# Kernel tuning notes

Measured on AMD Instinct MI355X. Metric: run time of the kernel, lower is better.

## Reference

```python
import jax, jax.numpy as jnp
import numpy as np

N_NODES = 100000
N_EDGES = 1600000
D_FEAT = 64
D_HID = 128
N_HOP = 3


def setup_inputs() -> dict:
    key = jax.random.key(0)
    ks = jax.random.split(key, 7)
    nodes = jax.random.normal(ks[0], (N_NODES, D_FEAT), dtype=jnp.float32)
    senders = jax.random.randint(ks[1], (N_EDGES,), 0, N_NODES, dtype=jnp.int32)
    receivers = jax.random.randint(ks[2], (N_EDGES,), 0, N_NODES, dtype=jnp.int32)
    # per-hop MLP params (n_hop=3 independent layers), lecun-style scaling
    W1 = jax.random.normal(ks[3], (N_HOP, D_FEAT, D_HID), dtype=jnp.float32) / np.sqrt(D_FEAT)
    b1 = jnp.zeros((N_HOP, D_HID), dtype=jnp.float32)
    W2 = jax.random.normal(ks[4], (N_HOP, D_HID, D_FEAT), dtype=jnp.float32) / np.sqrt(D_HID)
    b2 = jnp.zeros((N_HOP, D_FEAT), dtype=jnp.float32)
    return {"nodes": nodes, "senders": senders, "receivers": receivers,
            "W1": W1, "b1": b1, "W2": W2, "b2": b2}


def _gcn_hop(x, senders, receivers, w1, b1, w2, b2):
    # update_node_fn: 2-layer MLP with leaky_relu between layers
    x = jax.nn.leaky_relu(jnp.dot(x, w1) + b1)
    x = jnp.dot(x, w2) + b2
    n = x.shape[0]
    ones = jnp.ones(senders.shape, dtype=x.dtype)
    send_deg = jax.ops.segment_sum(ones, senders, num_segments=n)
    recv_deg = jax.ops.segment_sum(ones, receivers, num_segments=n)
    # symmetric normalization: D_s^{-1/2} gather -> scatter-sum -> D_r^{-1/2}
    x = x * jax.lax.rsqrt(jnp.maximum(send_deg, 1.0))[:, None]
    x = jax.ops.segment_sum(x[senders], receivers, num_segments=n)
    x = x * jax.lax.rsqrt(jnp.maximum(recv_deg, 1.0))[:, None]
    return x


def reference(nodes, senders, receivers, W1, b1, W2, b2):
    x = nodes
    for i in range(N_HOP):
        x = _gcn_hop(x, senders, receivers, W1[i], b1[i], W2[i], b2[i])
    return x
```

## Files before the change

kernel.cpp:

```cpp
#include <hip/hip_runtime.h>

#define LRELU_SLOPE 0.01f
#define NBLK_A 512
#define BIN_SZ 256
#define MAXBIN 5120
#define NC2 128

typedef unsigned short ushort_t;
typedef unsigned int uint_t;

typedef float f32x4 __attribute__((ext_vector_type(4)));
typedef short bf16x8 __attribute__((ext_vector_type(8)));
#define MFMA16(a, b, c) __builtin_amdgcn_mfma_f32_16x16x32_bf16(a, b, c, 0, 0, 0)

__device__ inline uint_t f2bf(float f) {
    unsigned u = __float_as_uint(f);
    return (u + 0x7FFFu + ((u >> 16) & 1u)) >> 16;
}

__device__ inline void split2(float v, uint_t& hi, uint_t& lo) {
    hi = f2bf(v);
    float hif = __uint_as_float(hi << 16);
    lo = f2bf(v - hif);
}

__device__ inline float4 bf4_to_f4(ushort4 v) {
    float4 r;
    r.x = __uint_as_float((unsigned)v.x << 16);
    r.y = __uint_as_float((unsigned)v.y << 16);
    r.z = __uint_as_float((unsigned)v.z << 16);
    r.w = __uint_as_float((unsigned)v.w << 16);
    return r;
}

__device__ inline void acc_bf8(uint4 v, float* a) {
    a[0] += __uint_as_float(v.x << 16);
    a[1] += __uint_as_float(v.x & 0xFFFF0000u);
    a[2] += __uint_as_float(v.y << 16);
    a[3] += __uint_as_float(v.y & 0xFFFF0000u);
    a[4] += __uint_as_float(v.z << 16);
    a[5] += __uint_as_float(v.z & 0xFFFF0000u);
    a[6] += __uint_as_float(v.w << 16);
    a[7] += __uint_as_float(v.w & 0xFFFF0000u);
}

__device__ inline void acc_bf8m(uint4 v, float ok, float* a) {
    a[0] = fmaf(__uint_as_float(v.x << 16), ok, a[0]);
    a[1] = fmaf(__uint_as_float(v.x & 0xFFFF0000u), ok, a[1]);
    a[2] = fmaf(__uint_as_float(v.y << 16), ok, a[2]);
    a[3] = fmaf(__uint_as_float(v.y & 0xFFFF0000u), ok, a[3]);
    a[4] = fmaf(__uint_as_float(v.z << 16), ok, a[4]);
    a[5] = fmaf(__uint_as_float(v.z & 0xFFFF0000u), ok, a[5]);
    a[6] = fmaf(__uint_as_float(v.w << 16), ok, a[6]);
    a[7] = fmaf(__uint_as_float(v.w & 0xFFFF0000u), ok, a[7]);
}


__global__ __launch_bounds__(256) void binhist_kernel(const int* __restrict__ keys,
        int* __restrict__ cntA, int cs, int e, int nbins) {
    __shared__ int cnt[512];
    int b = blockIdx.x, t = threadIdx.x;
    for (int i = t; i < nbins; i += 256) cnt[i] = 0;
    __syncthreads();
    int base = b * cs, lim = min(cs, e - base);
    for (int i = t; i < lim; i += 256)
        atomicAdd(&cnt[keys[base + i] >> 8], 1);
    __syncthreads();
    for (int i = t; i < nbins; i += 256) cntA[b * nbins + i] = cnt[i];
}

__global__ __launch_bounds__(512) void binoffA_kernel(const int* __restrict__ cntA,
        int* __restrict__ offT, int* __restrict__ binTot, int nbins) {
    __shared__ int s[NBLK_A];
    int bin = blockIdx.x, t = threadIdx.x;
    int v = cntA[t * nbins + bin];
    s[t] = v;
    __syncthreads();
    for (int off = 1; off < NBLK_A; off <<= 1) {
        int add = (t >= off) ? s[t - off] : 0;
        __syncthreads();
        s[t] += add;
        __syncthreads();
    }
    offT[bin * NBLK_A + t] = s[t] - v;
    if (t == NBLK_A - 1) binTot[bin] = s[t];
}

__global__ __launch_bounds__(512) void scanb_kernel(const int* __restrict__ binTot,
        int* __restrict__ binStart, int nbins) {
    __shared__ int s[512];
    int t = threadIdx.x;
    int v = (t < nbins) ? binTot[t] : 0;
    s[t] = v;
    __syncthreads();
    for (int off = 1; off < 512; off <<= 1) {
        int add = (t >= off) ? s[t - off] : 0;
        __syncthreads();
        s[t] += add;
        __syncthreads();
    }
    if (t < nbins) binStart[t] = s[t] - v;
    if (t == nbins - 1) binStart[nbins] = s[t];
}

__global__ __launch_bounds__(256) void binscat_kernel(const int* __restrict__ keys,
        const int* __restrict__ payload, const int* __restrict__ offT,
        const int* __restrict__ binStart,
        uint2* __restrict__ pairs, int cs, int e, int nbins) {
    __shared__ int cur[512];
    int b = blockIdx.x, t = threadIdx.x;
    for (int i = t; i < nbins; i += 256) cur[i] = offT[i * NBLK_A + b] + binStart[i];
    __syncthreads();
    int base = b * cs, lim = min(cs, e - base);
    for (int i = t; i < lim; i += 256) {
        int k = keys[base + i];
        int pl = payload[base + i];
        int pos = atomicAdd(&cur[k >> 8], 1);
        pairs[pos] = make_uint2((unsigned)k, (unsigned)pl);
    }
}

__global__ __launch_bounds__(256) void binsort_kernel(const uint2* __restrict__ pairs,
        const int* __restrict__ binStart, int* __restrict__ row_start,
        int* __restrict__ bucket, int nbins, int n, int e) {
    __shared__ int cnt[BIN_SZ];
    __shared__ int loc[BIN_SZ];
    __shared__ int buf[MAXBIN];
    int bin = blockIdx.x, t = threadIdx.x;
    int e0 = binStart[bin], e1 = binStart[bin + 1];
    int m = e1 - e0;
    if (m > MAXBIN) m = MAXBIN;
    cnt[t] = 0;
    __syncthreads();
    for (int i = t; i < m; i += 256)
        atomicAdd(&cnt[pairs[e0 + i].x & 255], 1);
    __syncthreads();
    int v = cnt[t];
    int node = bin * BIN_SZ + t;
    loc[t] = v;
    __syncthreads();
    for (int off = 1; off < BIN_SZ; off <<= 1) {
        int add = (t >= off) ? loc[t - off] : 0;
        __syncthreads();
        loc[t] += add;
        __syncthreads();
    }
    int excl = loc[t] - v;
    if (node < n) row_start[node] = e0 + excl;
    if (bin == nbins - 1 && t == 255) row_start[n] = e;
    cnt[t] = excl;
    __syncthreads();
    for (int i = t; i < m; i += 256) {
        uint2 pr = pairs[e0 + i];
        int pos = atomicAdd(&cnt[pr.x & 255], 1);
        buf[pos] = (int)pr.y;
    }
    __syncthreads();
    for (int i = t; i < m; i += 256) bucket[e0 + i] = buf[i];
}


__global__ __launch_bounds__(256) void hist8v2_kernel(const int* __restrict__ keys,
        uint_t* __restrict__ hist, int cs, int e, int half, int nwords) {
    __shared__ uint_t lds[12500];
    int c = blockIdx.x >> 1;
    int h = blockIdx.x & 1;
    int t = threadIdx.x;
    int hw = half >> 2;
    for (int i = t; i < hw; i += 256) lds[i] = 0;
    __syncthreads();
    int base = c * cs, lim = min(cs, e - base);
    int lo = h * half;
    for (int i = t; i < lim; i += 256) {
        int v = keys[base + i] - lo;
        if ((unsigned)v < (unsigned)half)
            atomicAdd(&lds[v >> 2], 1u << ((v & 3) * 8));
    }
    __syncthreads();
    uint_t* d = hist + (size_t)c * nwords + (size_t)h * hw;
    for (int i = t; i < hw; i += 256) d[i] = lds[i];
}

__global__ __launch_bounds__(256) void scancv2_kernel(const uint_t* __restrict__ hist,
        int* __restrict__ deg, int nwords, int n) {
    int w = blockIdx.x * 256 + threadIdx.x;
    if (w >= nwords) return;
    uint_t run = 0;
    for (int c = 0; c < NC2; c++) run += hist[(size_t)c * nwords + w];
    int v = w * 4;
    if (v + 3 < n) {
        ((int4*)deg)[w] = make_int4(run & 255, (run >> 8) & 255,
                                    (run >> 16) & 255, (int)(run >> 24));
    } else {
        for (int j = 0; j < 4 && v + j < n; j++) deg[v + j] = (run >> (8 * j)) & 255;
    }
}


__global__ __launch_bounds__(256) void prep_w_kernel(const float* __restrict__ W1,
        const float* __restrict__ W2, ushort_t* __restrict__ w1p, ushort_t* __restrict__ w2p) {
    int hop = blockIdx.x;
    const float* w1 = W1 + hop * 64 * 128;
    const float* w2 = W2 + hop * 128 * 64;
    ushort_t* p1h = w1p + (size_t)hop * 16384;
    ushort_t* p1l = p1h + 8192;
    ushort_t* p2h = w2p + (size_t)hop * 16384;
    ushort_t* p2l = p2h + 8192;
    for (int i = threadIdx.x; i < 8192; i += 256) {
        int j = i & 7, o = (i >> 3) & 127, cq = i >> 10;
        int k = (cq >> 2) * 32 + (cq & 3) * 8 + j;
        uint_t h, l;
        split2(w1[k * 128 + o], h, l);
        p1h[i] = (ushort_t)h; p1l[i] = (ushort_t)l;
    }
    for (int i = threadIdx.x; i < 8192; i += 256) {
        int j = i & 7, o = (i >> 3) & 63, cq = i >> 9;
        int k = (cq >> 2) * 32 + (cq & 3) * 8 + j;
        uint_t h, l;
        split2(w2[k * 64 + o], h, l);
        p2h[i] = (ushort_t)h; p2l[i] = (ushort_t)l;
    }
}


template<int GATHER>
__global__ __launch_bounds__(512) void fused_mlp_kernel(const float* __restrict__ x,
        const ushort_t* __restrict__ yin, const int* __restrict__ rs,
        const int* __restrict__ bucket,
        const ushort_t* __restrict__ w1p, const float* __restrict__ b1g,
        const ushort_t* __restrict__ w2p, const float* __restrict__ b2g,
        const int* __restrict__ sdeg, ushort_t* __restrict__ y, int n) {
    __shared__ __align__(16) char smem[54272];
    ushort_t* xsh = (ushort_t*)smem;
    ushort_t* xsl = xsh + 4608;
    ushort_t* hsh = xsl + 4608;
    ushort_t* hsl = hsh + 8704;
    float* b1f   = (float*)(hsl + 8704);
    float* b2f   = b1f + 128;
    float* snorm = b2f + 64;
    float* ybuf  = (float*)smem;

    const ushort_t* w1ph = w1p;
    const ushort_t* w1pl = w1p + 8192;
    const ushort_t* w2ph = w2p;
    const ushort_t* w2pl = w2p + 8192;

    int tid = threadIdx.x;
    int nb = blockIdx.x * 64;

    if (tid < 32) ((float4*)b1f)[tid] = ((const float4*)b1g)[tid];
    else if (tid < 48) ((float4*)b2f)[tid - 32] = ((const float4*)b2g)[tid - 32];
    if (tid >= 448) {
        int t = tid - 448;
        int gn = nb + t;
        int d = (gn < n) ? sdeg[gn] : 1;
        snorm[t] = rsqrtf(fmaxf((float)d, 1.0f));
    }

    if (GATHER) {
        int node = tid >> 3, j = tid & 7;
        int gn = nb + node;
        float a[8];
        #pragma unroll
        for (int k = 0; k < 8; k++) a[k] = 0.f;
        if (gn < n) {
            int s0 = rs[gn];
            int deg = rs[gn + 1] - s0;
            const uint4* yrow = (const uint4*)yin;
            int i = 0;
            for (; i + 16 <= deg; i += 16) {
                int idx[16];
                #pragma unroll
                for (int k = 0; k < 16; k++) idx[k] = bucket[s0 + i + k];
                uint4 r0[16];
                #pragma unroll
                for (int k = 0; k < 16; k++) r0[k] = yrow[(size_t)idx[k] * 8 + j];
                #pragma unroll
                for (int k = 0; k < 16; k++) acc_bf8(r0[k], a);
            }
            for (; i < deg; i += 8) {
                int idx[8]; float ok[8];
                #pragma unroll
                for (int k = 0; k < 8; k++) {
                    int ii = i + k;
                    bool v = ii < deg;
                    idx[k] = bucket[v ? s0 + ii : s0];
                    ok[k] = v ? 1.0f : 0.0f;
                }
                uint4 rr[8];
                #pragma unroll
                for (int k = 0; k < 8; k++) rr[k] = yrow[(size_t)idx[k] * 8 + j];
                #pragma unroll
                for (int k = 0; k < 8; k++) acc_bf8m(rr[k], ok[k], a);
            }
            float sc = rsqrtf(fmaxf((float)deg, 1.0f));
            #pragma unroll
            for (int k = 0; k < 8; k++) a[k] *= sc;
        }
        uint_t h[8], l[8];
        #pragma unroll
        for (int k = 0; k < 8; k++) split2(a[k], h[k], l[k]);
        uint4 oh, ol;
        oh.x = h[0] | (h[1] << 16); oh.y = h[2] | (h[3] << 16);
        oh.z = h[4] | (h[5] << 16); oh.w = h[6] | (h[7] << 16);
        ol.x = l[0] | (l[1] << 16); ol.y = l[2] | (l[3] << 16);
        ol.z = l[4] | (l[5] << 16); ol.w = l[6] | (l[7] << 16);
        *(uint4*)&xsh[node * 72 + j * 8] = oh;
        *(uint4*)&xsl[node * 72 + j * 8] = ol;
    } else {
        for (int i = tid; i < 1024; i += 512) {
            int node = i >> 4, c4 = i & 15;
            int gn = nb + node;
            float4 v = make_float4(0.f, 0.f, 0.f, 0.f);
            if (gn < n) v = ((const float4*)x)[(size_t)gn * 16 + c4];
            uint_t h0, l0, h1, l1, h2, l2, h3, l3;
            split2(v.x, h0, l0); split2(v.y, h1, l1);
            split2(v.z, h2, l2); split2(v.w, h3, l3);
            *(uint2*)&xsh[node * 72 + c4 * 4] = make_uint2(h0 | (h1 << 16), h2 | (h3 << 16));
            *(uint2*)&xsl[node * 72 + c4 * 4] = make_uint2(l0 | (l1 << 16), l2 | (l3 << 16));
        }
    }
    __syncthreads();

    int w = tid >> 6, lane = tid & 63;
    int q = lane >> 4, m = lane & 15;
    int oq = w & 3, nh = w >> 2;
    bool even = ((m & 1) == 0);

    {
        f32x4 acc[2][2];
        #pragma unroll
        for (int a = 0; a < 2; a++)
            #pragma unroll
            for (int b = 0; b < 2; b++) acc[a][b] = (f32x4)(0.f);

        #pragma unroll
        for (int c = 0; c < 2; c++) {
            bf16x8 Ah[2], Al[2];
            #pragma unroll
            for (int nt = 0; nt < 2; nt++) {
                int node = nh * 32 + nt * 16 + m;
                Ah[nt] = *(const bf16x8*)&xsh[node * 72 + c * 32 + q * 8];
                Al[nt] = *(const bf16x8*)&xsl[node * 72 + c * 32 + q * 8];
            }
            #pragma unroll
            for (int ot = 0; ot < 2; ot++) {
                int o1 = oq * 32 + ot * 16 + m;
                size_t fo = (size_t)((c * 4 + q) * 128 + o1) * 8;
                bf16x8 Bh = *(const bf16x8*)&w1ph[fo];
                bf16x8 Bl = *(const bf16x8*)&w1pl[fo];
                #pragma unroll
                for (int nt = 0; nt < 2; nt++) {
                    acc[ot][nt] = MFMA16(Ah[nt], Bh, acc[ot][nt]);
                    acc[ot][nt] = MFMA16(Ah[nt], Bl, acc[ot][nt]);
                    acc[ot][nt] = MFMA16(Al[nt], Bh, acc[ot][nt]);
                }
            }
        }
        float b1v[2];
        b1v[0] = b1f[oq * 32 + m];
        b1v[1] = b1f[oq * 32 + 16 + m];
        #pragma unroll
        for (int ot = 0; ot < 2; ot++)
            #pragma unroll
            for (int nt = 0; nt < 2; nt++) {
                float hv[4], pv[4];
                #pragma unroll
                for (int r = 0; r < 4; r++) {
                    float t = acc[ot][nt][r] + b1v[ot];
                    hv[r] = (t > 0.f) ? t : LRELU_SLOPE * t;
                }
                #pragma unroll
                for (int r = 0; r < 4; r++) pv[r] = __shfl_xor(hv[r], 1, 64);
                int kpos = oq * 32 + ot * 16 + (m & ~1);
                #pragma unroll
                for (int rr = 0; rr < 2; rr++) {
                    int r = even ? rr : (2 + rr);
                    float vlo = even ? hv[r] : pv[r];
                    float vhi = even ? pv[r] : hv[r];
                    uint_t ah, al, bh, bl;
                    split2(vlo, ah, al);
                    split2(vhi, bh, bl);
                    int node = nh * 32 + nt * 16 + 4 * q + r;
                    *(uint_t*)&hsh[node * 136 + kpos] = ah | (bh << 16);
                    *(uint_t*)&hsl[node * 136 + kpos] = al | (bl << 16);
                }
            }
    }
    __syncthreads();

    {
        int ot2 = oq;
        f32x4 acc2[2];
        acc2[0] = (f32x4)(0.f);
        acc2[1] = (f32x4)(0.f);
        #pragma unroll
        for (int c = 0; c < 4; c++) {
            int o2 = ot2 * 16 + m;
            size_t fo = (size_t)((c * 4 + q) * 64 + o2) * 8;
            bf16x8 Bh = *(const bf16x8*)&w2ph[fo];
            bf16x8 Bl = *(const bf16x8*)&w2pl[fo];
            #pragma unroll
            for (int nt = 0; nt < 2; nt++) {
                int node = nh * 32 + nt * 16 + m;
                bf16x8 Ah = *(const bf16x8*)&hsh[node * 136 + c * 32 + q * 8];
                bf16x8 Al = *(const bf16x8*)&hsl[node * 136 + c * 32 + q * 8];
                acc2[nt] = MFMA16(Ah, Bh, acc2[nt]);
                acc2[nt] = MFMA16(Ah, Bl, acc2[nt]);
                acc2[nt] = MFMA16(Al, Bh, acc2[nt]);
            }
        }
        float b2v = b2f[ot2 * 16 + m];
        #pragma unroll
        for (int nt = 0; nt < 2; nt++)
            #pragma unroll
            for (int r = 0; r < 4; r++) {
                int node = nh * 32 + nt * 16 + 4 * q + r;
                float sn = snorm[node];
                ybuf[node * 68 + ot2 * 16 + m] = (acc2[nt][r] + b2v) * sn;
            }
    }
    __syncthreads();

    {
        int node = tid >> 3, c8 = tid & 7;
        int gn = nb + node;
        if (gn < n) {
            const float* src = &ybuf[node * 68 + c8 * 8];
            float4 v0 = *(const float4*)src;
            float4 v1 = *(const float4*)(src + 4);
            uint4 o;
            o.x = f2bf(v0.x) | (f2bf(v0.y) << 16);
            o.y = f2bf(v0.z) | (f2bf(v0.w) << 16);
            o.z = f2bf(v1.x) | (f2bf(v1.y) << 16);
            o.w = f2bf(v1.z) | (f2bf(v1.w) << 16);
            ((uint4*)y)[(size_t)gn * 8 + c8] = o;
        }
    }
}


__global__ __launch_bounds__(256) void agg_kernel(const ushort_t* __restrict__ y,
        const int* __restrict__ rs, const int* __restrict__ bucket,
        float* __restrict__ dst, int n) {
    int wid  = (blockIdx.x * 256 + threadIdx.x) >> 6;
    int lane = threadIdx.x & 63;
    int nd   = lane >> 5;
    int slot = (lane >> 4) & 1;
    int f4   = lane & 15;
    int node = wid * 2 + nd;
    if (node >= n) return;
    int s0  = rs[node];
    int deg = rs[node + 1] - s0;
    const ushort4* y4 = (const ushort4*)y;
    float4 acc = make_float4(0.f, 0.f, 0.f, 0.f);
    for (int i = slot; i < deg; i += 16) {
        int idx[8]; float ok[8];
        #pragma unroll
        for (int j = 0; j < 8; j++) {
            int ii = i + 2 * j;
            bool v = ii < deg;
            idx[j] = bucket[v ? s0 + ii : s0];
            ok[j] = v ? 1.0f : 0.0f;
        }
        #pragma unroll
        for (int j = 0; j < 8; j++) {
            float4 v4 = bf4_to_f4(y4[(size_t)idx[j] * 16 + f4]);
            acc.x = fmaf(v4.x, ok[j], acc.x);
            acc.y = fmaf(v4.y, ok[j], acc.y);
            acc.z = fmaf(v4.z, ok[j], acc.z);
            acc.w = fmaf(v4.w, ok[j], acc.w);
        }
    }
    acc.x += __shfl_xor(acc.x, 16, 64);
    acc.y += __shfl_xor(acc.y, 16, 64);
    acc.z += __shfl_xor(acc.z, 16, 64);
    acc.w += __shfl_xor(acc.w, 16, 64);
    if (slot == 0) {
        float sc = rsqrtf(fmaxf((float)deg, 1.0f));
        acc.x *= sc; acc.y *= sc; acc.z *= sc; acc.w *= sc;
        ((float4*)dst)[(size_t)node * 16 + f4] = acc;
    }
}


extern "C" void kernel_launch(void* const* d_in, const int* in_sizes, int n_in,
                              void* d_out, int out_size, void* d_ws, size_t ws_size,
                              hipStream_t stream) {
    const float* nodes     = (const float*)d_in[0];
    const int*   senders   = (const int*)d_in[1];
    const int*   receivers = (const int*)d_in[2];
    const float* W1 = (const float*)d_in[3];
    const float* b1 = (const float*)d_in[4];
    const float* W2 = (const float*)d_in[5];
    const float* b2 = (const float*)d_in[6];

    int N = in_sizes[0] / 64;
    int E = in_sizes[1];
    int NBINS = (N + BIN_SZ - 1) / BIN_SZ;
    int CSA = (E + NBLK_A - 1) / NBLK_A;
    int CS2 = (E + NC2 - 1) / NC2;
    int HALF = ((N + 7) / 8) * 4;
    int NW2 = 2 * (HALF >> 2);

    char* p = (char*)d_ws;
    auto carve = [&](size_t bytes) -> char* {
        char* r = p;
        p += (bytes + 255) & ~(size_t)255;
        return r;
    };
    ushort_t* yA   = (ushort_t*)carve((size_t)N * 64 * 2);
    ushort_t* yB   = (ushort_t*)carve((size_t)N * 64 * 2);
    int*      rs   = (int*)carve((size_t)(N + 1) * 4);
    int*      sdeg = (int*)carve((size_t)N * 4);
    int*      bucket = (int*)carve((size_t)E * 4);
    int*      binStart = (int*)carve((size_t)(NBINS + 1) * 4);
    int*      binTot   = (int*)carve((size_t)NBINS * 4);
    ushort_t* w1p  = (ushort_t*)carve((size_t)3 * 16384 * 2);
    ushort_t* w2p  = (ushort_t*)carve((size_t)3 * 16384 * 2);
    char* scratch  = carve((size_t)E * 8 + 2 * (size_t)NBLK_A * NBINS * 4 + 4096);
    uint2* pairs = (uint2*)scratch;
    int*   cntA  = (int*)(scratch + (size_t)E * 8);
    int*   offT  = cntA + (size_t)NBLK_A * NBINS;
    uint_t* T1   = (uint_t*)pairs;

    prep_w_kernel<<<3, 256, 0, stream>>>(W1, W2, w1p, w2p);
    binhist_kernel<<<NBLK_A, 256, 0, stream>>>(receivers, cntA, CSA, E, NBINS);
    binoffA_kernel<<<NBINS, NBLK_A, 0, stream>>>(cntA, offT, binTot, NBINS);
    scanb_kernel<<<1, 512, 0, stream>>>(binTot, binStart, NBINS);
    binscat_kernel<<<NBLK_A, 256, 0, stream>>>(receivers, senders, offT, binStart, pairs, CSA, E, NBINS);
    binsort_kernel<<<NBINS, 256, 0, stream>>>(pairs, binStart, rs, bucket, NBINS, N, E);
    hist8v2_kernel<<<NC2 * 2, 256, 0, stream>>>(senders, T1, CS2, E, HALF, NW2);
    scancv2_kernel<<<(NW2 + 255) / 256, 256, 0, stream>>>(T1, sdeg, NW2, N);

    int mbf = (N + 63) / 64;
    int agg_blocks = (N / 2 + 4) / 4 + 1;

    fused_mlp_kernel<0><<<mbf, 512, 0, stream>>>(nodes, nullptr, nullptr, nullptr,
            w1p, b1, w2p, b2, sdeg, yA, N);
    fused_mlp_kernel<1><<<mbf, 512, 0, stream>>>(nullptr, yA, rs, bucket,
            w1p + 16384, b1 + 128, w2p + 16384, b2 + 64, sdeg, yB, N);
    fused_mlp_kernel<1><<<mbf, 512, 0, stream>>>(nullptr, yB, rs, bucket,
            w1p + 32768, b1 + 256, w2p + 32768, b2 + 128, sdeg, yA, N);
    agg_kernel<<<agg_blocks, 256, 0, stream>>>(yA, rs, bucket, (float*)d_out, N);
}
```

Baseline: 358.1 us.

## Merge preprocessing kernels and software-pipeline gather with MLP over two node tiles

The weight-prep, receiver bin histogram and sender degree histogram kernels are merged into one launch, and the bin-offset scan and degree reduction into a second, which cuts the number of small launches. The gather+MLP hops now run in a new kernel that handles two 64-node tiles per block. The first 16 neighbour rows of the second tile are prefetched while the first tile's MFMA work runs, so gather latency overlaps with compute. This raises register pressure (the 16 prefetched uint4 registers) and halves the grid size, with launch bounds set to 4 blocks.

```diff
diff --git a/kernel.cpp b/kernel.cpp
--- a/kernel.cpp
+++ b/kernel.cpp
@@ -56,34 +56,100 @@
 }
 
 
-__global__ __launch_bounds__(256) void binhist_kernel(const int* __restrict__ keys,
-        int* __restrict__ cntA, int cs, int e, int nbins) {
-    __shared__ int cnt[512];
-    int b = blockIdx.x, t = threadIdx.x;
-    for (int i = t; i < nbins; i += 256) cnt[i] = 0;
-    __syncthreads();
-    int base = b * cs, lim = min(cs, e - base);
-    for (int i = t; i < lim; i += 256)
-        atomicAdd(&cnt[keys[base + i] >> 8], 1);
-    __syncthreads();
-    for (int i = t; i < nbins; i += 256) cntA[b * nbins + i] = cnt[i];
-}
-
-__global__ __launch_bounds__(512) void binoffA_kernel(const int* __restrict__ cntA,
-        int* __restrict__ offT, int* __restrict__ binTot, int nbins) {
+__global__ __launch_bounds__(256) void build1_kernel(
+        const float* __restrict__ W1, const float* __restrict__ W2,
+        ushort_t* __restrict__ w1p, ushort_t* __restrict__ w2p,
+        const int* __restrict__ receivers, int* __restrict__ cntA, int csA,
+        const int* __restrict__ senders, uint_t* __restrict__ hist, int cs2,
+        int e, int nbins, int half, int nwords) {
+    __shared__ uint_t lds[12544];
+    int bid = blockIdx.x, t = threadIdx.x;
+    if (bid < 3) {
+        int hop = bid;
+        const float* w1 = W1 + hop * 64 * 128;
+        const float* w2 = W2 + hop * 128 * 64;
+        ushort_t* p1h = w1p + (size_t)hop * 16384;
+        ushort_t* p1l = p1h + 8192;
+        ushort_t* p2h = w2p + (size_t)hop * 16384;
+        ushort_t* p2l = p2h + 8192;
+        for (int i = t; i < 8192; i += 256) {
+            int j = i & 7, o = (i >> 3) & 127, cq = i >> 10;
+            int k = (cq >> 2) * 32 + (cq & 3) * 8 + j;
+            uint_t h, l;
+            split2(w1[k * 128 + o], h, l);
+            p1h[i] = (ushort_t)h; p1l[i] = (ushort_t)l;
+        }
+        for (int i = t; i < 8192; i += 256) {
+            int j = i & 7, o = (i >> 3) & 63, cq = i >> 9;
+            int k = (cq >> 2) * 32 + (cq & 3) * 8 + j;
+            uint_t h, l;
+            split2(w2[k * 64 + o], h, l);
+            p2h[i] = (ushort_t)h; p2l[i] = (ushort_t)l;
+        }
+    } else if (bid < 3 + NBLK_A) {
+        int* cnt = (int*)lds;
+        int b = bid - 3;
+        for (int i = t; i < nbins; i += 256) cnt[i] = 0;
+        __syncthreads();
+        int base = b * csA, lim = min(csA, e - base);
+        for (int i = t; i < lim; i += 256)
+            atomicAdd(&cnt[receivers[base + i] >> 8], 1);
+        __syncthreads();
+        for (int i = t; i < nbins; i += 256) cntA[b * nbins + i] = cnt[i];
+    } else {
+        int idx = bid - 3 - NBLK_A;
+        int c = idx >> 1;
+        int h = idx & 1;
+        int hw = half >> 2;
+        for (int i = t; i < hw; i += 256) lds[i] = 0;
+        __syncthreads();
+        int base = c * cs2, lim = min(cs2, e - base);
+        int lo = h * half;
+        for (int i = t; i < lim; i += 256) {
+            int v = senders[base + i] - lo;
+            if ((unsigned)v < (unsigned)half)
+                atomicAdd(&lds[v >> 2], 1u << ((v & 3) * 8));
+        }
+        __syncthreads();
+        uint_t* d = hist + (size_t)c * nwords + (size_t)h * hw;
+        for (int i = t; i < hw; i += 256) d[i] = lds[i];
+    }
+}
+
+
+__global__ __launch_bounds__(512) void build2_kernel(
+        const int* __restrict__ cntA, int* __restrict__ offT,
+        int* __restrict__ binTot, int nbins,
+        const uint_t* __restrict__ hist, int* __restrict__ deg,
+        int nwords, int n) {
     __shared__ int s[NBLK_A];
-    int bin = blockIdx.x, t = threadIdx.x;
-    int v = cntA[t * nbins + bin];
-    s[t] = v;
-    __syncthreads();
-    for (int off = 1; off < NBLK_A; off <<= 1) {
-        int add = (t >= off) ? s[t - off] : 0;
+    int bid = blockIdx.x, t = threadIdx.x;
+    if (bid < nbins) {
+        int bin = bid;
+        int v = cntA[t * nbins + bin];
+        s[t] = v;
         __syncthreads();
-        s[t] += add;
-        __syncthreads();
-    }
-    offT[bin * NBLK_A + t] = s[t] - v;
-    if (t == NBLK_A - 1) binTot[bin] = s[t];
+        for (int off = 1; off < NBLK_A; off <<= 1) {
+            int add = (t >= off) ? s[t - off] : 0;
+            __syncthreads();
+            s[t] += add;
+            __syncthreads();
+        }
+        offT[bin * NBLK_A + t] = s[t] - v;
+        if (t == NBLK_A - 1) binTot[bin] = s[t];
+    } else {
+        int w = (bid - nbins) * 512 + t;
+        if (w >= nwords) return;
+        uint_t run = 0;
+        for (int c = 0; c < NC2; c++) run += hist[(size_t)c * nwords + w];
+        int v = w * 4;
+        if (v + 3 < n) {
+            ((int4*)deg)[w] = make_int4(run & 255, (run >> 8) & 255,
+                                        (run >> 16) & 255, (int)(run >> 24));
+        } else {
+            for (int j = 0; j < 4 && v + j < n; j++) deg[v + j] = (run >> (8 * j)) & 255;
+        }
+    }
 }
 
 __global__ __launch_bounds__(512) void scanb_kernel(const int* __restrict__ binTot,
@@ -160,73 +226,8 @@
 }
 
 
-__global__ __launch_bounds__(256) void hist8v2_kernel(const int* __restrict__ keys,
-        uint_t* __restrict__ hist, int cs, int e, int half, int nwords) {
-    __shared__ uint_t lds[12500];
-    int c = blockIdx.x >> 1;
-    int h = blockIdx.x & 1;
-    int t = threadIdx.x;
-    int hw = half >> 2;
-    for (int i = t; i < hw; i += 256) lds[i] = 0;
-    __syncthreads();
-    int base = c * cs, lim = min(cs, e - base);
-    int lo = h * half;
-    for (int i = t; i < lim; i += 256) {
-        int v = keys[base + i] - lo;
-        if ((unsigned)v < (unsigned)half)
-            atomicAdd(&lds[v >> 2], 1u << ((v & 3) * 8));
-    }
-    __syncthreads();
-    uint_t* d = hist + (size_t)c * nwords + (size_t)h * hw;
-    for (int i = t; i < hw; i += 256) d[i] = lds[i];
-}
-
-__global__ __launch_bounds__(256) void scancv2_kernel(const uint_t* __restrict__ hist,
-        int* __restrict__ deg, int nwords, int n) {
-    int w = blockIdx.x * 256 + threadIdx.x;
-    if (w >= nwords) return;
-    uint_t run = 0;
-    for (int c = 0; c < NC2; c++) run += hist[(size_t)c * nwords + w];
-    int v = w * 4;
-    if (v + 3 < n) {
-        ((int4*)deg)[w] = make_int4(run & 255, (run >> 8) & 255,
-                                    (run >> 16) & 255, (int)(run >> 24));
-    } else {
-        for (int j = 0; j < 4 && v + j < n; j++) deg[v + j] = (run >> (8 * j)) & 255;
-    }
-}
-
-
-__global__ __launch_bounds__(256) void prep_w_kernel(const float* __restrict__ W1,
-        const float* __restrict__ W2, ushort_t* __restrict__ w1p, ushort_t* __restrict__ w2p) {
-    int hop = blockIdx.x;
-    const float* w1 = W1 + hop * 64 * 128;
-    const float* w2 = W2 + hop * 128 * 64;
-    ushort_t* p1h = w1p + (size_t)hop * 16384;
-    ushort_t* p1l = p1h + 8192;
-    ushort_t* p2h = w2p + (size_t)hop * 16384;
-    ushort_t* p2l = p2h + 8192;
-    for (int i = threadIdx.x; i < 8192; i += 256) {
-        int j = i & 7, o = (i >> 3) & 127, cq = i >> 10;
-        int k = (cq >> 2) * 32 + (cq & 3) * 8 + j;
-        uint_t h, l;
-        split2(w1[k * 128 + o], h, l);
-        p1h[i] = (ushort_t)h; p1l[i] = (ushort_t)l;
-    }
-    for (int i = threadIdx.x; i < 8192; i += 256) {
-        int j = i & 7, o = (i >> 3) & 63, cq = i >> 9;
-        int k = (cq >> 2) * 32 + (cq & 3) * 8 + j;
-        uint_t h, l;
-        split2(w2[k * 64 + o], h, l);
-        p2h[i] = (ushort_t)h; p2l[i] = (ushort_t)l;
-    }
-}
-
-
 template<int GATHER>
 __global__ __launch_bounds__(512) void fused_mlp_kernel(const float* __restrict__ x,
-        const ushort_t* __restrict__ yin, const int* __restrict__ rs,
-        const int* __restrict__ bucket,
         const ushort_t* __restrict__ w1p, const float* __restrict__ b1g,
         const ushort_t* __restrict__ w2p, const float* __restrict__ b2g,
         const int* __restrict__ sdeg, ushort_t* __restrict__ y, int n) {
@@ -257,68 +258,16 @@
         snorm[t] = rsqrtf(fmaxf((float)d, 1.0f));
     }
 
-    if (GATHER) {
-        int node = tid >> 3, j = tid & 7;
+    for (int i = tid; i < 1024; i += 512) {
+        int node = i >> 4, c4 = i & 15;
         int gn = nb + node;
-        float a[8];
-        #pragma unroll
-        for (int k = 0; k < 8; k++) a[k] = 0.f;
-        if (gn < n) {
-            int s0 = rs[gn];
-            int deg = rs[gn + 1] - s0;
-            const uint4* yrow = (const uint4*)yin;
-            int i = 0;
-            for (; i + 16 <= deg; i += 16) {
-                int idx[16];
-                #pragma unroll
-                for (int k = 0; k < 16; k++) idx[k] = bucket[s0 + i + k];
-                uint4 r0[16];
-                #pragma unroll
-                for (int k = 0; k < 16; k++) r0[k] = yrow[(size_t)idx[k] * 8 + j];
-                #pragma unroll
-                for (int k = 0; k < 16; k++) acc_bf8(r0[k], a);
-            }
-            for (; i < deg; i += 8) {
-                int idx[8]; float ok[8];
-                #pragma unroll
-                for (int k = 0; k < 8; k++) {
-                    int ii = i + k;
-                    bool v = ii < deg;
-                    idx[k] = bucket[v ? s0 + ii : s0];
-                    ok[k] = v ? 1.0f : 0.0f;
-                }
-                uint4 rr[8];
-                #pragma unroll
-                for (int k = 0; k < 8; k++) rr[k] = yrow[(size_t)idx[k] * 8 + j];
-                #pragma unroll
-                for (int k = 0; k < 8; k++) acc_bf8m(rr[k], ok[k], a);
-            }
-            float sc = rsqrtf(fmaxf((float)deg, 1.0f));
-            #pragma unroll
-            for (int k = 0; k < 8; k++) a[k] *= sc;
-        }
-        uint_t h[8], l[8];
-        #pragma unroll
-        for (int k = 0; k < 8; k++) split2(a[k], h[k], l[k]);
-        uint4 oh, ol;
-        oh.x = h[0] | (h[1] << 16); oh.y = h[2] | (h[3] << 16);
-        oh.z = h[4] | (h[5] << 16); oh.w = h[6] | (h[7] << 16);
-        ol.x = l[0] | (l[1] << 16); ol.y = l[2] | (l[3] << 16);
-        ol.z = l[4] | (l[5] << 16); ol.w = l[6] | (l[7] << 16);
-        *(uint4*)&xsh[node * 72 + j * 8] = oh;
-        *(uint4*)&xsl[node * 72 + j * 8] = ol;
-    } else {
-        for (int i = tid; i < 1024; i += 512) {
-            int node = i >> 4, c4 = i & 15;
-            int gn = nb + node;
-            float4 v = make_float4(0.f, 0.f, 0.f, 0.f);
-            if (gn < n) v = ((const float4*)x)[(size_t)gn * 16 + c4];
-            uint_t h0, l0, h1, l1, h2, l2, h3, l3;
-            split2(v.x, h0, l0); split2(v.y, h1, l1);
-            split2(v.z, h2, l2); split2(v.w, h3, l3);
-            *(uint2*)&xsh[node * 72 + c4 * 4] = make_uint2(h0 | (h1 << 16), h2 | (h3 << 16));
-            *(uint2*)&xsl[node * 72 + c4 * 4] = make_uint2(l0 | (l1 << 16), l2 | (l3 << 16));
-        }
+        float4 v = make_float4(0.f, 0.f, 0.f, 0.f);
+        if (gn < n) v = ((const float4*)x)[(size_t)gn * 16 + c4];
+        uint_t h0, l0, h1, l1, h2, l2, h3, l3;
+        split2(v.x, h0, l0); split2(v.y, h1, l1);
+        split2(v.z, h2, l2); split2(v.w, h3, l3);
+        *(uint2*)&xsh[node * 72 + c4 * 4] = make_uint2(h0 | (h1 << 16), h2 | (h3 << 16));
+        *(uint2*)&xsl[node * 72 + c4 * 4] = make_uint2(l0 | (l1 << 16), l2 | (l3 << 16));
     }
     __syncthreads();
 
@@ -427,6 +376,380 @@
         int gn = nb + node;
         if (gn < n) {
             const float* src = &ybuf[node * 68 + c8 * 8];
+            float4 v0 = *(const float4*)src;
+            float4 v1 = *(const float4*)(src + 4);
+            uint4 o;
+            o.x = f2bf(v0.x) | (f2bf(v0.y) << 16);
+            o.y = f2bf(v0.z) | (f2bf(v0.w) << 16);
+            o.z = f2bf(v1.x) | (f2bf(v1.y) << 16);
+            o.w = f2bf(v1.z) | (f2bf(v1.w) << 16);
+            ((uint4*)y)[(size_t)gn * 8 + c8] = o;
+        }
+    }
+}
+
+
+__global__ __launch_bounds__(512, 4) void fused_mlp2_kernel(
+        const ushort_t* __restrict__ yin, const int* __restrict__ rs,
+        const int* __restrict__ bucket,
+        const ushort_t* __restrict__ w1p, const float* __restrict__ b1g,
+        const ushort_t* __restrict__ w2p, const float* __restrict__ b2g,
+        const int* __restrict__ sdeg, ushort_t* __restrict__ y, int n) {
+    __shared__ __align__(16) char smem[54528];
+    ushort_t* xsh = (ushort_t*)smem;
+    ushort_t* xsl = xsh + 4608;
+    ushort_t* hsh = xsl + 4608;
+    ushort_t* hsl = hsh + 8704;
+    float* b1f = (float*)(hsl + 8704);
+    float* b2f = b1f + 128;
+    float* snA = b2f + 64;
+    float* snB = snA + 64;
+    float* ybuf = (float*)smem;
+
+    const ushort_t* w1ph = w1p;
+    const ushort_t* w1pl = w1p + 8192;
+    const ushort_t* w2ph = w2p;
+    const ushort_t* w2pl = w2p + 8192;
+    const uint4* yrow = (const uint4*)yin;
+
+    int tid = threadIdx.x;
+    int nbA = blockIdx.x * 128;
+    int nbB = nbA + 64;
+
+    if (tid < 32) ((float4*)b1f)[tid] = ((const float4*)b1g)[tid];
+    else if (tid < 48) ((float4*)b2f)[tid - 32] = ((const float4*)b2g)[tid - 32];
+    if (tid >= 448) {
+        int t = tid - 448;
+        int gn = nbA + t;
+        int d = (gn < n) ? sdeg[gn] : 1;
+        snA[t] = rsqrtf(fmaxf((float)d, 1.0f));
+    } else if (tid >= 384) {
+        int t = tid - 384;
+        int gn = nbB + t;
+        int d = (gn < n) ? sdeg[gn] : 1;
+        snB[t] = rsqrtf(fmaxf((float)d, 1.0f));
+    }
+
+    int node = tid >> 3, j = tid & 7;
+
+    int gnB = nbB + node;
+    int s0B = 0, degB = 0;
+    if (gnB < n) {
+        s0B = rs[gnB];
+        degB = rs[gnB + 1] - s0B;
+    }
+    int idxB[16];
+    #pragma unroll
+    for (int k = 0; k < 16; k++)
+        idxB[k] = bucket[(k < degB) ? s0B + k : s0B];
+
+    {
+        int gn = nbA + node;
+        float a[8];
+        #pragma unroll
+        for (int k = 0; k < 8; k++) a[k] = 0.f;
+        if (gn < n) {
+            int s0 = rs[gn];
+            int deg = rs[gn + 1] - s0;
+            int i = 0;
+            for (; i + 16 <= deg; i += 16) {
+                int idx[16];
+                #pragma unroll
+                for (int k = 0; k < 16; k++) idx[k] = bucket[s0 + i + k];
+                uint4 r0[16];
+                #pragma unroll
+                for (int k = 0; k < 16; k++) r0[k] = yrow[(size_t)idx[k] * 8 + j];
+                #pragma unroll
+                for (int k = 0; k < 16; k++) acc_bf8(r0[k], a);
+            }
+            for (; i < deg; i += 8) {
+                int idx[8]; float ok[8];
+                #pragma unroll
+                for (int k = 0; k < 8; k++) {
+                    int ii = i + k;
+                    bool v = ii < deg;
+                    idx[k] = bucket[v ? s0 + ii : s0];
+                    ok[k] = v ? 1.0f : 0.0f;
+                }
+                uint4 rr[8];
+                #pragma unroll
+                for (int k = 0; k < 8; k++) rr[k] = yrow[(size_t)idx[k] * 8 + j];
+                #pragma unroll
+                for (int k = 0; k < 8; k++) acc_bf8m(rr[k], ok[k], a);
+            }
+            float sc = rsqrtf(fmaxf((float)deg, 1.0f));
+            #pragma unroll
+            for (int k = 0; k < 8; k++) a[k] *= sc;
+        }
+        uint_t h[8], l[8];
+        #pragma unroll
+        for (int k = 0; k < 8; k++) split2(a[k], h[k], l[k]);
+        uint4 oh, ol;
+        oh.x = h[0] | (h[1] << 16); oh.y = h[2] | (h[3] << 16);
+        oh.z = h[4] | (h[5] << 16); oh.w = h[6] | (h[7] << 16);
+        ol.x = l[0] | (l[1] << 16); ol.y = l[2] | (l[3] << 16);
+        ol.z = l[4] | (l[5] << 16); ol.w = l[6] | (l[7] << 16);
+        *(uint4*)&xsh[node * 72 + j * 8] = oh;
+        *(uint4*)&xsl[node * 72 + j * 8] = ol;
+    }
+    __syncthreads();
+
+    uint4 rB[16];
+    #pragma unroll
+    for (int k = 0; k < 16; k++) rB[k] = yrow[(size_t)idxB[k] * 8 + j];
+
+    int w = tid >> 6, lane = tid & 63;
+    int q = lane >> 4, m = lane & 15;
+    int oq = w & 3, nh = w >> 2;
+    bool even = ((m & 1) == 0);
+
+    {
+        f32x4 acc[2][2];
+        #pragma unroll
+        for (int a = 0; a < 2; a++)
+            #pragma unroll
+            for (int b = 0; b < 2; b++) acc[a][b] = (f32x4)(0.f);
+        #pragma unroll
+        for (int c = 0; c < 2; c++) {
+            bf16x8 Ah[2], Al[2];
+            #pragma unroll
+            for (int nt = 0; nt < 2; nt++) {
+                int nd = nh * 32 + nt * 16 + m;
+                Ah[nt] = *(const bf16x8*)&xsh[nd * 72 + c * 32 + q * 8];
+                Al[nt] = *(const bf16x8*)&xsl[nd * 72 + c * 32 + q * 8];
+            }
+            #pragma unroll
+            for (int ot = 0; ot < 2; ot++) {
+                int o1 = oq * 32 + ot * 16 + m;
+                size_t fo = (size_t)((c * 4 + q) * 128 + o1) * 8;
+                bf16x8 Bh = *(const bf16x8*)&w1ph[fo];
+                bf16x8 Bl = *(const bf16x8*)&w1pl[fo];
+                #pragma unroll
+                for (int nt = 0; nt < 2; nt++) {
+                    acc[ot][nt] = MFMA16(Ah[nt], Bh, acc[ot][nt]);
+                    acc[ot][nt] = MFMA16(Ah[nt], Bl, acc[ot][nt]);
+                    acc[ot][nt] = MFMA16(Al[nt], Bh, acc[ot][nt]);
+                }
+            }
+        }
+        float b1v[2];
+        b1v[0] = b1f[oq * 32 + m];
+        b1v[1] = b1f[oq * 32 + 16 + m];
+        #pragma unroll
+        for (int ot = 0; ot < 2; ot++)
+            #pragma unroll
+            for (int nt = 0; nt < 2; nt++) {
+                float hv[4], pv[4];
+                #pragma unroll
+                for (int r = 0; r < 4; r++) {
+                    float t = acc[ot][nt][r] + b1v[ot];
+                    hv[r] = (t > 0.f) ? t : LRELU_SLOPE * t;
+                }
+                #pragma unroll
+                for (int r = 0; r < 4; r++) pv[r] = __shfl_xor(hv[r], 1, 64);
+                int kpos = oq * 32 + ot * 16 + (m & ~1);
+                #pragma unroll
+                for (int rr = 0; rr < 2; rr++) {
+                    int r = even ? rr : (2 + rr);
+                    float vlo = even ? hv[r] : pv[r];
+                    float vhi = even ? pv[r] : hv[r];
+                    uint_t ah, al, bh, bl;
+                    split2(vlo, ah, al);
+                    split2(vhi, bh, bl);
+                    int nd = nh * 32 + nt * 16 + 4 * q + r;
+                    *(uint_t*)&hsh[nd * 136 + kpos] = ah | (bh << 16);
+                    *(uint_t*)&hsl[nd * 136 + kpos] = al | (bl << 16);
+                }
+            }
+    }
+    __syncthreads();
+
+    float aB[8];
+    #pragma unroll
+    for (int k = 0; k < 8; k++) aB[k] = 0.f;
+    #pragma unroll
+    for (int k = 0; k < 16; k++)
+        acc_bf8m(rB[k], (k < degB) ? 1.0f : 0.0f, aB);
+
+    {
+        int ot2 = oq;
+        f32x4 acc2[2];
+        acc2[0] = (f32x4)(0.f);
+        acc2[1] = (f32x4)(0.f);
+        #pragma unroll
+        for (int c = 0; c < 4; c++) {
+            int o2 = ot2 * 16 + m;
+            size_t fo = (size_t)((c * 4 + q) * 64 + o2) * 8;
+            bf16x8 Bh = *(const bf16x8*)&w2ph[fo];
+            bf16x8 Bl = *(const bf16x8*)&w2pl[fo];
+            #pragma unroll
+            for (int nt = 0; nt < 2; nt++) {
+                int nd = nh * 32 + nt * 16 + m;
+                bf16x8 Ah = *(const bf16x8*)&hsh[nd * 136 + c * 32 + q * 8];
+                bf16x8 Al = *(const bf16x8*)&hsl[nd * 136 + c * 32 + q * 8];
+                acc2[nt] = MFMA16(Ah, Bh, acc2[nt]);
+                acc2[nt] = MFMA16(Ah, Bl, acc2[nt]);
+                acc2[nt] = MFMA16(Al, Bh, acc2[nt]);
+            }
+        }
+        float b2v = b2f[ot2 * 16 + m];
+        #pragma unroll
+        for (int nt = 0; nt < 2; nt++)
+            #pragma unroll
+            for (int r = 0; r < 4; r++) {
+                int nd = nh * 32 + nt * 16 + 4 * q + r;
+                ybuf[nd * 68 + ot2 * 16 + m] = (acc2[nt][r] + b2v) * snA[nd];
+            }
+    }
+    __syncthreads();
+
+    {
+        int nd = tid >> 3, c8 = tid & 7;
+        int gn = nbA + nd;
+        if (gn < n) {
+            const float* src = &ybuf[nd * 68 + c8 * 8];
+            float4 v0 = *(const float4*)src;
+            float4 v1 = *(const float4*)(src + 4);
+            uint4 o;
+            o.x = f2bf(v0.x) | (f2bf(v0.y) << 16);
+            o.y = f2bf(v0.z) | (f2bf(v0.w) << 16);
+            o.z = f2bf(v1.x) | (f2bf(v1.y) << 16);
+            o.w = f2bf(v1.z) | (f2bf(v1.w) << 16);
+            ((uint4*)y)[(size_t)gn * 8 + c8] = o;
+        }
+    }
+    __syncthreads();
+
+    {
+        for (int i = 16; i < degB; i += 8) {
+            int idx[8]; float ok[8];
+            #pragma unroll
+            for (int k = 0; k < 8; k++) {
+                int ii = i + k;
+                bool v = ii < degB;
+                idx[k] = bucket[v ? s0B + ii : s0B];
+                ok[k] = v ? 1.0f : 0.0f;
+            }
+            uint4 rr[8];
+            #pragma unroll
+            for (int k = 0; k < 8; k++) rr[k] = yrow[(size_t)idx[k] * 8 + j];
+            #pragma unroll
+            for (int k = 0; k < 8; k++) acc_bf8m(rr[k], ok[k], aB);
+        }
+        float sc = rsqrtf(fmaxf((float)degB, 1.0f));
+        #pragma unroll
+        for (int k = 0; k < 8; k++) aB[k] *= sc;
+        uint_t h[8], l[8];
+        #pragma unroll
+        for (int k = 0; k < 8; k++) split2(aB[k], h[k], l[k]);
+        uint4 oh, ol;
+        oh.x = h[0] | (h[1] << 16); oh.y = h[2] | (h[3] << 16);
+        oh.z = h[4] | (h[5] << 16); oh.w = h[6] | (h[7] << 16);
+        ol.x = l[0] | (l[1] << 16); ol.y = l[2] | (l[3] << 16);
+        ol.z = l[4] | (l[5] << 16); ol.w = l[6] | (l[7] << 16);
+        *(uint4*)&xsh[node * 72 + j * 8] = oh;
+        *(uint4*)&xsl[node * 72 + j * 8] = ol;
+    }
+    __syncthreads();
+
+    {
+        f32x4 acc[2][2];
+        #pragma unroll
+        for (int a = 0; a < 2; a++)
+            #pragma unroll
+            for (int b = 0; b < 2; b++) acc[a][b] = (f32x4)(0.f);
+        #pragma unroll
+        for (int c = 0; c < 2; c++) {
+            bf16x8 Ah[2], Al[2];
+            #pragma unroll
+            for (int nt = 0; nt < 2; nt++) {
+                int nd = nh * 32 + nt * 16 + m;
+                Ah[nt] = *(const bf16x8*)&xsh[nd * 72 + c * 32 + q * 8];
+                Al[nt] = *(const bf16x8*)&xsl[nd * 72 + c * 32 + q * 8];
+            }
+            #pragma unroll
+            for (int ot = 0; ot < 2; ot++) {
+                int o1 = oq * 32 + ot * 16 + m;
+                size_t fo = (size_t)((c * 4 + q) * 128 + o1) * 8;
+                bf16x8 Bh = *(const bf16x8*)&w1ph[fo];
+                bf16x8 Bl = *(const bf16x8*)&w1pl[fo];
+                #pragma unroll
+                for (int nt = 0; nt < 2; nt++) {
+                    acc[ot][nt] = MFMA16(Ah[nt], Bh, acc[ot][nt]);
+                    acc[ot][nt] = MFMA16(Ah[nt], Bl, acc[ot][nt]);
+                    acc[ot][nt] = MFMA16(Al[nt], Bh, acc[ot][nt]);
+                }
+            }
+        }
+        float b1v[2];
+        b1v[0] = b1f[oq * 32 + m];
+        b1v[1] = b1f[oq * 32 + 16 + m];
+        #pragma unroll
+        for (int ot = 0; ot < 2; ot++)
+            #pragma unroll
+            for (int nt = 0; nt < 2; nt++) {
+                float hv[4], pv[4];
+                #pragma unroll
+                for (int r = 0; r < 4; r++) {
+                    float t = acc[ot][nt][r] + b1v[ot];
+                    hv[r] = (t > 0.f) ? t : LRELU_SLOPE * t;
+                }
+                #pragma unroll
+                for (int r = 0; r < 4; r++) pv[r] = __shfl_xor(hv[r], 1, 64);
+                int kpos = oq * 32 + ot * 16 + (m & ~1);
+                #pragma unroll
+                for (int rr = 0; rr < 2; rr++) {
+                    int r = even ? rr : (2 + rr);
+                    float vlo = even ? hv[r] : pv[r];
+                    float vhi = even ? pv[r] : hv[r];
+                    uint_t ah, al, bh, bl;
+                    split2(vlo, ah, al);
+                    split2(vhi, bh, bl);
+                    int nd = nh * 32 + nt * 16 + 4 * q + r;
+                    *(uint_t*)&hsh[nd * 136 + kpos] = ah | (bh << 16);
+                    *(uint_t*)&hsl[nd * 136 + kpos] = al | (bl << 16);
+                }
+            }
+    }
+    __syncthreads();
+
+    {
+        int ot2 = oq;
+        f32x4 acc2[2];
+        acc2[0] = (f32x4)(0.f);
+        acc2[1] = (f32x4)(0.f);
+        #pragma unroll
+        for (int c = 0; c < 4; c++) {
+            int o2 = ot2 * 16 + m;
+            size_t fo = (size_t)((c * 4 + q) * 64 + o2) * 8;
+            bf16x8 Bh = *(const bf16x8*)&w2ph[fo];
+            bf16x8 Bl = *(const bf16x8*)&w2pl[fo];
+            #pragma unroll
+            for (int nt = 0; nt < 2; nt++) {
+                int nd = nh * 32 + nt * 16 + m;
+                bf16x8 Ah = *(const bf16x8*)&hsh[nd * 136 + c * 32 + q * 8];
+                bf16x8 Al = *(const bf16x8*)&hsl[nd * 136 + c * 32 + q * 8];
+                acc2[nt] = MFMA16(Ah, Bh, acc2[nt]);
+                acc2[nt] = MFMA16(Ah, Bl, acc2[nt]);
+                acc2[nt] = MFMA16(Al, Bh, acc2[nt]);
+            }
+        }
+        float b2v = b2f[ot2 * 16 + m];
+        #pragma unroll
+        for (int nt = 0; nt < 2; nt++)
+            #pragma unroll
+            for (int r = 0; r < 4; r++) {
+                int nd = nh * 32 + nt * 16 + 4 * q + r;
+                ybuf[nd * 68 + ot2 * 16 + m] = (acc2[nt][r] + b2v) * snB[nd];
+            }
+    }
+    __syncthreads();
+
+    {
+        int nd = tid >> 3, c8 = tid & 7;
+        int gn = nbB + nd;
+        if (gn < n) {
+            const float* src = &ybuf[nd * 68 + c8 * 8];
             float4 v0 = *(const float4*)src;
             float4 v1 = *(const float4*)(src + 4);
             uint4 o;
@@ -524,23 +847,24 @@
     int*   offT  = cntA + (size_t)NBLK_A * NBINS;
     uint_t* T1   = (uint_t*)pairs;
 
-    prep_w_kernel<<<3, 256, 0, stream>>>(W1, W2, w1p, w2p);
-    binhist_kernel<<<NBLK_A, 256, 0, stream>>>(receivers, cntA, CSA, E, NBINS);
-    binoffA_kernel<<<NBINS, NBLK_A, 0, stream>>>(cntA, offT, binTot, NBINS);
+    build1_kernel<<<3 + NBLK_A + NC2 * 2, 256, 0, stream>>>(
+            W1, W2, w1p, w2p, receivers, cntA, CSA,
+            senders, T1, CS2, E, NBINS, HALF, NW2);
+    build2_kernel<<<NBINS + (NW2 + 511) / 512, 512, 0, stream>>>(
+            cntA, offT, binTot, NBINS, T1, sdeg, NW2, N);
     scanb_kernel<<<1, 512, 0, stream>>>(binTot, binStart, NBINS);
     binscat_kernel<<<NBLK_A, 256, 0, stream>>>(receivers, senders, offT, binStart, pairs, CSA, E, NBINS);
     binsort_kernel<<<NBINS, 256, 0, stream>>>(pairs, binStart, rs, bucket, NBINS, N, E);
-    hist8v2_kernel<<<NC2 * 2, 256, 0, stream>>>(senders, T1, CS2, E, HALF, NW2);
-    scancv2_kernel<<<(NW2 + 255) / 256, 256, 0, stream>>>(T1, sdeg, NW2, N);
-
-    int mbf = (N + 63) / 64;
+
+    int mbf  = (N + 63) / 64;
+    int mbf2 = (N + 127) / 128;
     int agg_blocks = (N / 2 + 4) / 4 + 1;
 
-    fused_mlp_kernel<0><<<mbf, 512, 0, stream>>>(nodes, nullptr, nullptr, nullptr,
+    fused_mlp_kernel<0><<<mbf, 512, 0, stream>>>(nodes,
             w1p, b1, w2p, b2, sdeg, yA, N);
-    fused_mlp_kernel<1><<<mbf, 512, 0, stream>>>(nullptr, yA, rs, bucket,
+    fused_mlp2_kernel<<<mbf2, 512, 0, stream>>>(yA, rs, bucket,
             w1p + 16384, b1 + 128, w2p + 16384, b2 + 64, sdeg, yB, N);
-    fused_mlp_kernel<1><<<mbf, 512, 0, stream>>>(nullptr, yB, rs, bucket,
+    fused_mlp2_kernel<<<mbf2, 512, 0, stream>>>(yB, rs, bucket,
             w1p + 32768, b1 + 256, w2p + 32768, b2 + 128, sdeg, yA, N);
     agg_kernel<<<agg_blocks, 256, 0, stream>>>(yA, rs, bucket, (float*)d_out, N);
 }
```

Result: slower. 371.0 us (+3.6%).
